# Optimization experiments

Hardware: AMD Instinct MI355X
Metric: run time of the kernel (lower is better)

Reference implementation:

```python
import jax, jax.numpy as jnp
import numpy as np

D = 512       # d_model
H = 8         # n_heads
HD = D // H   # head_dim = 64
BS = 64       # block_size
B = 1
S = 8192
NB = S // BS  # 128 blocks
THRESH = 0.3


def setup_inputs() -> dict:
    key = jax.random.key(0)
    ks = jax.random.split(key, 6)
    sc = 0.02
    return {
        "x": jax.random.normal(ks[0], (B, S, D), jnp.float32),
        "w_qkv": (jax.random.normal(ks[1], (D, 3 * D)) * sc).astype(jnp.float32),
        "b_qkv": jnp.zeros((3 * D,), jnp.float32),
        "w_out": (jax.random.normal(ks[2], (D, D)) * sc).astype(jnp.float32),
        "b_out": jnp.zeros((D,), jnp.float32),
        "w_r1": (jax.random.normal(ks[3], (D, 128)) * sc).astype(jnp.float32),
        "b_r1": jnp.zeros((128,), jnp.float32),
        "w_r2": (jax.random.normal(ks[4], (128, 1)) * sc).astype(jnp.float32),
        "b_r2": jnp.full((1,), 0.5, jnp.float32),  # sigmoid(~0.5)>0.3 -> non-degenerate mask
    }


def reference(x, w_qkv, b_qkv, w_out, b_out, w_r1, b_r1, w_r2, b_r2):
    Bx, Sx, Dx = x.shape
    qkv = (x @ w_qkv + b_qkv).reshape(Bx, Sx, 3, H, HD)
    q = jnp.transpose(qkv[:, :, 0], (0, 2, 1, 3))  # [B,H,S,HD]
    k = jnp.transpose(qkv[:, :, 1], (0, 2, 1, 3))
    v = jnp.transpose(qkv[:, :, 2], (0, 2, 1, 3))

    # --- router: per-block importance from mean-pooled q block (d_model features) ---
    qb = q.reshape(Bx, H, NB, BS, HD)
    rep = jnp.transpose(qb.mean(axis=3), (0, 2, 1, 3)).reshape(Bx, NB, Dx)  # [B,NB,D]
    imp = jax.nn.sigmoid(jax.nn.relu(rep @ w_r1 + b_r1) @ w_r2 + b_r2)[..., 0]  # [B,NB]
    keep = (imp.mean(axis=0) >= THRESH).astype(x.dtype)  # [NB], shared across batch (torch uses batch-mean)

    kb = k.reshape(Bx, H, NB, BS, HD)
    vb = v.reshape(Bx, H, NB, BS, HD)
    tri = jnp.triu(jnp.ones((BS, BS), bool), 1)  # strict upper triangle within diagonal block
    jidx = jnp.arange(NB)
    scale = 1.0 / np.sqrt(HD)

    def step(carry, i):
        q_i = jax.lax.dynamic_slice_in_dim(q, i * BS, BS, axis=2)        # [B,H,BSq,HD]
        s = jnp.einsum('bhqd,bhjkd->bhqjk', q_i, kb) * scale             # [B,H,BSq,NB,BSk]
        causal = (jidx == i)[None, :, None] & tri[:, None, :]            # [BSq,NB,BSk]
        s = jnp.where(causal[None, None], -jnp.inf, s)
        p = jax.nn.softmax(s, axis=-1)                                   # softmax PER key-block (as in torch loop)
        wj = keep * keep[i]                                              # block pair gate [NB]
        o = jnp.einsum('bhqjk,j,bhjkd->bhqd', p, wj, vb)                 # sum of gated per-block contributions
        return carry, o

    _, outs = jax.lax.scan(step, None, jnp.arange(NB))                   # [NB,B,H,BSq,HD]
    attn = jnp.transpose(outs, (1, 2, 0, 3, 4)).reshape(Bx, H, Sx, HD)
    attn = jnp.transpose(attn, (0, 2, 1, 3)).reshape(Bx, Sx, Dx)
    return attn @ w_out + b_out
```

## Files before the change

kernel.cpp:

```cpp
#include <hip/hip_runtime.h>

typedef unsigned short u16;
typedef unsigned int u32;
typedef __attribute__((ext_vector_type(8))) short short8;
typedef __attribute__((ext_vector_type(4))) short short4v;
typedef __attribute__((ext_vector_type(4))) float f32x4;
typedef __attribute__((ext_vector_type(4))) float float4v;
typedef __attribute__((ext_vector_type(2))) u32 u32x2;
typedef __attribute__((ext_vector_type(4))) u32 u32x4;

#define S_LEN 8192
#define NHEAD 8
#define NBLK  128
#define SCALE_C 0.18033688011112042f

__device__ __forceinline__ u16 f2b(float f) {
    union { float f; unsigned u; } v; v.f = f;
    unsigned r = v.u + 0x7FFFu + ((v.u >> 16) & 1u);
    return (u16)(r >> 16);
}
__device__ __forceinline__ float b2f(u16 b) {
    union { float f; unsigned u; } v; v.u = ((unsigned)b) << 16; return v.f;
}
__device__ __forceinline__ u32 cvt_pk_bf16(float lo, float hi) {
    u32 r;
    asm("v_cvt_pk_bf16_f32 %0, %1, %2" : "=v"(r) : "v"(lo), "v"(hi));
    return r;
}
__device__ __forceinline__ void pl16swap(u32& a, u32& b) {
    u32x2 r = __builtin_amdgcn_permlane16_swap(a, b, false, false);
    a = r[0]; b = r[1];
}
__device__ __forceinline__ void pl32swap(u32& a, u32& b) {
    u32x2 r = __builtin_amdgcn_permlane32_swap(a, b, false, false);
    a = r[0]; b = r[1];
}
__device__ __forceinline__ int swz(int row, int colByte) {
    return row * 128 + (colByte ^ ((row & 7) << 4));
}
__device__ __forceinline__ void gload_lds(const void* g, void* l) {
    __builtin_amdgcn_global_load_lds(
        (const __attribute__((address_space(1))) void*)g,
        (__attribute__((address_space(3))) void*)l, 16, 0, 0);
}

__global__ __launch_bounds__(256) void cvt_x_kernel(const float* __restrict__ x, u16* __restrict__ xb) {
    int idx = blockIdx.x * 256 + threadIdx.x;
    float4v v = *((const float4v*)x + idx);
    short4v o;
    #pragma unroll
    for (int r = 0; r < 4; ++r) o[r] = (short)f2b(v[r]);
    *((short4v*)xb + idx) = o;
}

__global__ __launch_bounds__(256) void cvt_T_kernel(const float* __restrict__ w, u16* __restrict__ wt, int C) {
    int idx = blockIdx.x * 256 + threadIdx.x;
    int r = idx & 511, cc = idx >> 9;
    wt[idx] = f2b(w[(size_t)r * C + cc]);
}

__global__ __launch_bounds__(256) void sum4_kernel(const u16* __restrict__ a0, const u16* __restrict__ a1,
                                                   const u16* __restrict__ a2, const u16* __restrict__ a3,
                                                   int n, u16* __restrict__ outb) {
    int idx = blockIdx.x * 256 + threadIdx.x;
    short8 v0 = ((const short8*)a0)[idx];
    short8 v1 = ((const short8*)a1)[idx];
    float s[8];
    #pragma unroll
    for (int e = 0; e < 8; ++e) s[e] = b2f((u16)v0[e]) + b2f((u16)v1[e]);
    if (n == 4) {
        short8 v2 = ((const short8*)a2)[idx];
        short8 v3 = ((const short8*)a3)[idx];
        #pragma unroll
        for (int e = 0; e < 8; ++e) s[e] += b2f((u16)v2[e]) + b2f((u16)v3[e]);
    }
    short8 o;
    #pragma unroll
    for (int e = 0; e < 8; ++e) o[e] = (short)f2b(s[e]);
    ((short8*)outb)[idx] = o;
}

__device__ __forceinline__ void gemm128_core(const u16* __restrict__ A,
                                             const u16* __restrict__ Bt,
                                             int m0, int n0, char* As, char* Bs,
                                             f32x4 acc[4][4]) {
    const int tid = threadIdx.x;
    const int lane = tid & 63, wid = tid >> 6;
    const int q16 = lane >> 4, l16 = lane & 15;
    const int wm = wid >> 1, wn = wid & 1;
    #pragma unroll 1
    for (int kt = 0; kt < 8; ++kt) {
        const int k0 = kt * 64;
        __syncthreads();
        #pragma unroll
        for (int p = 0; p < 4; ++p) {
            int c = tid + p * 256;
            int row = c >> 3, colp = (c & 7) ^ (row & 7);
            gload_lds(A  + (size_t)(m0 + row) * 512 + k0 + colp * 8, As + (size_t)(wid * 64 + p * 256) * 16);
            gload_lds(Bt + (size_t)(n0 + row) * 512 + k0 + colp * 8, Bs + (size_t)(wid * 64 + p * 256) * 16);
        }
        __syncthreads();
        #pragma unroll
        for (int kk = 0; kk < 2; ++kk) {
            short8 a[4], b[4];
            #pragma unroll
            for (int t = 0; t < 4; ++t) {
                int arow = wm * 64 + t * 16 + l16;
                a[t] = *(const short8*)(As + swz(arow, kk * 64 + q16 * 16));
                int brow = wn * 64 + t * 16 + l16;
                b[t] = *(const short8*)(Bs + swz(brow, kk * 64 + q16 * 16));
            }
            #pragma unroll
            for (int mt = 0; mt < 4; ++mt)
                #pragma unroll
                for (int nt = 0; nt < 4; ++nt)
                    acc[mt][nt] = __builtin_amdgcn_mfma_f32_16x16x32_bf16(a[mt], b[nt], acc[mt][nt], 0, 0, 0);
        }
    }
}

__global__ __launch_bounds__(256) void qkv_gemm(const u16* __restrict__ xb, const u16* __restrict__ wqkvT,
                                                const float* __restrict__ bqkv,
                                                u16* __restrict__ qb, u16* __restrict__ kf, u16* __restrict__ vf) {
    __shared__ char smem[32768];
    f32x4 acc[4][4];
    #pragma unroll
    for (int a = 0; a < 4; ++a)
        #pragma unroll
        for (int b = 0; b < 4; ++b) acc[a][b] = (f32x4){0.f, 0.f, 0.f, 0.f};
    const int m0 = blockIdx.x * 128, n0 = blockIdx.y * 128;
    gemm128_core(xb, wqkvT, m0, n0, smem, smem + 16384, acc);

    const int lane = threadIdx.x & 63, wid = threadIdx.x >> 6;
    const int q16 = lane >> 4, l16 = lane & 15;
    const int wm = wid >> 1, wn = wid & 1;
    #pragma unroll
    for (int mt = 0; mt < 4; ++mt) {
        #pragma unroll
        for (int nt = 0; nt < 4; ++nt) {
            int n = n0 + wn * 64 + nt * 16 + l16;
            float bias = bqkv[n];
            int t = n >> 9, h = (n >> 6) & 7, d = n & 63;
            int sb = m0 + wm * 64 + mt * 16 + q16 * 4;
            f32x4 v = acc[mt][nt];
            if (t == 0) {
                #pragma unroll
                for (int r = 0; r < 4; ++r)
                    qb[(size_t)(h * S_LEN + sb + r) * 64 + d] = f2b((v[r] + bias) * SCALE_C);
            } else if (t == 1) {
                int j = sb >> 6, key = sb & 63;
                int n0k = key >> 4, c = d >> 5, q16k = (d >> 3) & 3, e = d & 7;
                int ub = (n0k * 2 + c) * 64 + q16k * 16 + (key & 15);
                u16* base = kf + (size_t)h * 524288 + (size_t)j * 4096 + e;
                #pragma unroll
                for (int r = 0; r < 4; ++r)
                    base[(ub + r) * 8] = f2b(v[r] + bias);
            } else {
                int j = sb >> 6, key = sb & 63;
                int dt = d >> 4, c = key >> 5, q16v = (key >> 3) & 3, e0 = key & 7;
                int u = (dt * 2 + c) * 64 + q16v * 16 + (d & 15);
                short4v pk;
                #pragma unroll
                for (int r = 0; r < 4; ++r) pk[r] = (short)f2b(v[r] + bias);
                *(short4v*)(vf + (size_t)h * 524288 + (size_t)j * 4096 + u * 8 + e0) = pk;
            }
        }
    }
}

__global__ __launch_bounds__(256) void out_gemm(const u16* __restrict__ a0, const u16* __restrict__ wotT,
                                                const float* __restrict__ bout, float* __restrict__ out) {
    __shared__ char smem[32768];
    f32x4 acc[4][4];
    #pragma unroll
    for (int a = 0; a < 4; ++a)
        #pragma unroll
        for (int b = 0; b < 4; ++b) acc[a][b] = (f32x4){0.f, 0.f, 0.f, 0.f};
    const int m0 = blockIdx.x * 128, n0 = blockIdx.y * 128;
    gemm128_core(a0, wotT, m0, n0, smem, smem + 16384, acc);

    const int lane = threadIdx.x & 63, wid = threadIdx.x >> 6;
    const int q16 = lane >> 4, l16 = lane & 15;
    const int wm = wid >> 1, wn = wid & 1;
    #pragma unroll
    for (int mt = 0; mt < 4; ++mt) {
        #pragma unroll
        for (int nt = 0; nt < 4; ++nt) {
            int n = n0 + wn * 64 + nt * 16 + l16;
            float bias = bout[n];
            int sb = m0 + wm * 64 + mt * 16 + q16 * 4;
            #pragma unroll
            for (int r = 0; r < 4; ++r)
                out[(size_t)(sb + r) * 512 + n] = acc[mt][nt][r] + bias;
        }
    }
}

__global__ __launch_bounds__(256) void router_kernel(const u16* __restrict__ qb,
                                                     const float* __restrict__ w_r1, const float* __restrict__ b_r1,
                                                     const float* __restrict__ w_r2, const float* __restrict__ b_r2,
                                                     float* __restrict__ keepf) {
    const int nb = blockIdx.x, tid = threadIdx.x;
    __shared__ float rep[512];
    __shared__ float h1[128];
    for (int dim = tid; dim < 512; dim += 256) {
        int h = dim >> 6, d = dim & 63;
        const u16* p = qb + (size_t)(h * S_LEN + nb * 64) * 64 + d;
        float s = 0.f;
        #pragma unroll 4
        for (int t = 0; t < 64; ++t) s += b2f(p[t * 64]);
        rep[dim] = s * (0.015625f / SCALE_C);
    }
    __syncthreads();
    if (tid < 128) {
        float a = b_r1[tid];
        for (int k = 0; k < 512; ++k) a += rep[k] * w_r1[k * 128 + tid];
        h1[tid] = fmaxf(a, 0.f);
    }
    __syncthreads();
    if (tid < 64) {
        float v = h1[tid] * w_r2[tid] + h1[tid + 64] * w_r2[tid + 64];
        #pragma unroll
        for (int off = 32; off; off >>= 1) v += __shfl_down(v, off);
        if (tid == 0) {
            float z = v + b_r2[0];
            keepf[nb] = (z >= -0.84729786f) ? 1.0f : 0.0f;
        }
    }
}

__global__ __launch_bounds__(256, 4) void attn_kernel(const u16* __restrict__ qb, const u16* __restrict__ kf,
                                                      const u16* __restrict__ vf, const float* __restrict__ keepf,
                                                      u16* __restrict__ a0, u16* __restrict__ a1,
                                                      u16* __restrict__ a2, u16* __restrict__ a3, int nj) {
    const int i = blockIdx.x, h = blockIdx.y, jh = blockIdx.z;
    const int j0 = jh * nj;
    u16* __restrict__ att = (jh == 0) ? a0 : (jh == 1) ? a1 : (jh == 2) ? a2 : a3;
    const int tid = threadIdx.x, lane = tid & 63, wid = tid >> 6;
    const int q16 = lane >> 4, l16 = lane & 15;
    __shared__ char smem[40960];

    short8 bq[2][2];
    #pragma unroll
    for (int qh = 0; qh < 2; ++qh) {
        const u16* qrow = qb + (size_t)(h * S_LEN + i * 128 + wid * 32 + qh * 16 + l16) * 64;
        bq[qh][0] = *(const short8*)(qrow + q16 * 8);
        bq[qh][1] = *(const short8*)(qrow + 32 + q16 * 8);
    }
    const int kq_s = __builtin_amdgcn_readfirstlane(i * 2 + (wid >> 1));
    const float keep_i = keepf[kq_s];
    const u32 kvbits = __builtin_bit_cast(u32, keepf[(j0 + lane) & 127]);
    const int qloc = (wid & 1) * 32 + l16;

    f32x4 o[2][4];
    #pragma unroll
    for (int qh = 0; qh < 2; ++qh)
        #pragma unroll
        for (int t = 0; t < 4; ++t) o[qh][t] = (f32x4){0.f, 0.f, 0.f, 0.f};

    const int lb = lane * 16;
    const int stoff = (wid * 128 + lane) * 8;
    const int ldw = wid * 2048;

    const u16* kst = kf + (size_t)h * 524288 + stoff + (size_t)j0 * 4096;
    const u16* vst = vf + (size_t)h * 524288 + stoff + (size_t)j0 * 4096;
    char *kRead = smem + 8192, *kStage = smem;
    char *vPV = smem + 16384, *vNext = smem + 24576, *vStage = smem + 32768;

    asm volatile("s_waitcnt vmcnt(0)" ::: "memory");

    auto STAGE = [&](char* kdst, char* vdst) {
        gload_lds(kst,       kdst + ldw);   gload_lds(kst + 512, kdst + ldw + 1024);
        gload_lds(vst,       vdst + ldw);   gload_lds(vst + 512, vdst + ldw + 1024);
        kst += 4096; vst += 4096;
    };
    auto QK = [&](const char* Kc, f32x4 (&s)[2][4]) {
        __builtin_amdgcn_s_setprio(1);
        #pragma unroll
        for (int n0 = 0; n0 < 4; ++n0) {
            short8 ka0 = *(const short8*)(Kc + n0 * 2048 + lb);
            short8 ka1 = *(const short8*)(Kc + n0 * 2048 + 1024 + lb);
            #pragma unroll
            for (int qh = 0; qh < 2; ++qh) {
                f32x4 a = (f32x4){0.f, 0.f, 0.f, 0.f};
                a = __builtin_amdgcn_mfma_f32_16x16x32_bf16(ka0, bq[qh][0], a, 0, 0, 0);
                a = __builtin_amdgcn_mfma_f32_16x16x32_bf16(ka1, bq[qh][1], a, 0, 0, 0);
                s[qh][n0] = a;
            }
        }
        __builtin_amdgcn_s_setprio(0);
    };
    auto SMPV = [&](int jjl, const f32x4 (&s)[2][4], const char* Vc) {
        const float kj = __builtin_bit_cast(float, (u32)__builtin_amdgcn_readlane((int)kvbits, jjl));
        const float gj = keep_i * kj;
        const int j = j0 + jjl;
        short8 pb[2][2];
        #pragma unroll
        for (int qh = 0; qh < 2; ++qh) {
            f32x4 p4[4];
            #pragma unroll
            for (int n0 = 0; n0 < 4; ++n0)
                #pragma unroll
                for (int r = 0; r < 4; ++r)
                    p4[n0][r] = __builtin_amdgcn_exp2f(s[qh][n0][r]);
            if (j == kq_s) {
                const int qthis = qloc + qh * 16;
                #pragma unroll
                for (int n0 = 0; n0 < 4; ++n0)
                    #pragma unroll
                    for (int r = 0; r < 4; ++r)
                        if (n0 * 16 + q16 * 4 + r > qthis) p4[n0][r] = 0.f;
            }
            f32x4 sv = (p4[0] + p4[1]) + (p4[2] + p4[3]);
            float sum = (sv[0] + sv[1]) + (sv[2] + sv[3]);
            {
                u32 sa = __builtin_bit_cast(u32, sum), sb = sa;
                pl16swap(sa, sb);
                sum = __builtin_bit_cast(float, sa) + __builtin_bit_cast(float, sb);
                u32 sc = __builtin_bit_cast(u32, sum), sd = sc;
                pl32swap(sc, sd);
                sum = __builtin_bit_cast(float, sc) + __builtin_bit_cast(float, sd);
            }
            const float rinv = gj * __builtin_amdgcn_rcpf(sum);
            u32 dw[4][2];
            #pragma unroll
            for (int n0 = 0; n0 < 4; ++n0) {
                f32x4 t = p4[n0] * rinv;
                dw[n0][0] = cvt_pk_bf16(t[0], t[1]);
                dw[n0][1] = cvt_pk_bf16(t[2], t[3]);
            }
            #pragma unroll
            for (int kk = 0; kk < 2; ++kk) {
                u32 c0 = dw[2 * kk][0], d0 = dw[2 * kk + 1][0];
                pl32swap(c0, d0);
                pl16swap(c0, d0);
                u32 c1 = dw[2 * kk][1], d1 = dw[2 * kk + 1][1];
                pl32swap(c1, d1);
                pl16swap(c1, d1);
                u32x4 wv;
                wv[0] = c0; wv[1] = c1; wv[2] = d0; wv[3] = d1;
                pb[qh][kk] = __builtin_bit_cast(short8, wv);
            }
        }
        __builtin_amdgcn_s_setprio(1);
        #pragma unroll
        for (int dt = 0; dt < 4; ++dt) {
            short8 va0 = *(const short8*)(Vc + dt * 2048 + lb);
            short8 va1 = *(const short8*)(Vc + dt * 2048 + 1024 + lb);
            #pragma unroll
            for (int qh = 0; qh < 2; ++qh) {
                o[qh][dt] = __builtin_amdgcn_mfma_f32_16x16x32_bf16(va0, pb[qh][0], o[qh][dt], 0, 0, 0);
                o[qh][dt] = __builtin_amdgcn_mfma_f32_16x16x32_bf16(va1, pb[qh][1], o[qh][dt], 0, 0, 0);
            }
        }
        __builtin_amdgcn_s_setprio(0);
    };
    auto WAITBAR = [&]() {
        asm volatile("s_waitcnt vmcnt(0)" ::: "memory");
        __builtin_amdgcn_s_barrier();
        __builtin_amdgcn_sched_barrier(0);
    };
    auto ROT = [&]() {
        char* t = kRead; kRead = kStage; kStage = t;
        char* u = vPV; vPV = vNext; vNext = vStage; vStage = u;
    };

    STAGE(kStage, vPV);
    STAGE(kRead, vNext);
    asm volatile("s_waitcnt vmcnt(4)" ::: "memory");
    __builtin_amdgcn_s_barrier();

    f32x4 sA[2][4], sB[2][4];
    QK(kStage, sA);

    for (int jj = 0; jj + 3 < nj; jj += 2) {
        WAITBAR();
        STAGE(kStage, vStage);
        QK(kRead, sB);
        SMPV(jj, sA, vPV);
        ROT();
        WAITBAR();
        STAGE(kStage, vStage);
        QK(kRead, sA);
        SMPV(jj + 1, sB, vPV);
        ROT();
    }
    WAITBAR();
    QK(kRead, sB);
    SMPV(nj - 2, sA, vPV);
    ROT();
    WAITBAR();
    SMPV(nj - 1, sB, vPV);

    #pragma unroll
    for (int qh = 0; qh < 2; ++qh) {
        u16* obase = att + (size_t)(i * 128 + wid * 32 + qh * 16 + l16) * 512 + h * 64 + q16 * 4;
        #pragma unroll
        for (int dt = 0; dt < 4; ++dt) {
            u32x2 st;
            st[0] = cvt_pk_bf16(o[qh][dt][0], o[qh][dt][1]);
            st[1] = cvt_pk_bf16(o[qh][dt][2], o[qh][dt][3]);
            *(u32x2*)(obase + dt * 16) = st;
        }
    }
}

static const size_t OFF_WQKVT = 0;
static const size_t OFF_WOTT  = (size_t)2u << 20;
static const size_t OFF_KEEP  = ((size_t)2u << 20) + (512u << 10);
static const size_t OFF_QB    = (size_t)3u << 20;
static const size_t OFF_KF    = (size_t)11u << 20;
static const size_t OFF_VF    = (size_t)19u << 20;
static const size_t OFF_XB    = (size_t)27u << 20;
static const size_t OFF_P0    = (size_t)35u << 20;
static const size_t OFF_P1    = (size_t)43u << 20;
static const size_t OFF_P2    = (size_t)51u << 20;

extern "C" void kernel_launch(void* const* d_in, const int* in_sizes, int n_in,
                              void* d_out, int out_size, void* d_ws, size_t ws_size,
                              hipStream_t stream) {
    const float* x     = (const float*)d_in[0];
    const float* w_qkv = (const float*)d_in[1];
    const float* b_qkv = (const float*)d_in[2];
    const float* w_out = (const float*)d_in[3];
    const float* b_out = (const float*)d_in[4];
    const float* w_r1  = (const float*)d_in[5];
    const float* b_r1  = (const float*)d_in[6];
    const float* w_r2  = (const float*)d_in[7];
    const float* b_r2  = (const float*)d_in[8];
    float* out = (float*)d_out;
    char* ws = (char*)d_ws;
    u16* wqkvT  = (u16*)(ws + OFF_WQKVT);
    u16* wotT   = (u16*)(ws + OFF_WOTT);
    float* keepf = (float*)(ws + OFF_KEEP);
    u16* qb     = (u16*)(ws + OFF_QB);
    u16* kf     = (u16*)(ws + OFF_KF);
    u16* vf     = (u16*)(ws + OFF_VF);
    u16* xb     = (u16*)(ws + OFF_XB);
    u16* attnb  = (u16*)(ws + OFF_QB);

    const bool big = ws_size >= ((size_t)59u << 20) + 4096;
    const int njh = big ? 4 : 2;
    const int nj  = NBLK / njh;
    u16* a0 = (u16*)(ws + OFF_P0);
    u16* a1 = big ? (u16*)(ws + OFF_P1) : (u16*)(ws + OFF_XB);
    u16* a2 = big ? (u16*)(ws + OFF_P2) : a0;
    u16* a3 = big ? (u16*)(ws + OFF_XB) : a0;

    cvt_x_kernel<<<4096, 256, 0, stream>>>(x, xb);
    cvt_T_kernel<<<3072, 256, 0, stream>>>(w_qkv, wqkvT, 1536);
    cvt_T_kernel<<<1024, 256, 0, stream>>>(w_out, wotT, 512);
    qkv_gemm<<<dim3(64, 12), 256, 0, stream>>>(xb, wqkvT, b_qkv, qb, kf, vf);
    router_kernel<<<128, 256, 0, stream>>>(qb, w_r1, b_r1, w_r2, b_r2, keepf);
    attn_kernel<<<dim3(64, 8, njh), 256, 0, stream>>>(qb, kf, vf, keepf, a0, a1, a2, a3, nj);
    sum4_kernel<<<2048, 256, 0, stream>>>(a0, a1, a2, a3, njh, attnb);
    out_gemm<<<dim3(64, 4), 256, 0, stream>>>(attnb, wotT, b_out, out);
}
```

Measured before the change: 240.5 us.

## Shrink attention LDS to 2-deep V ring, fix 2-way key split, vectorize router

The attention kernel now keeps two V buffers in LDS instead of three, cutting shared memory from 40KB to 32KB and raising the launch bound to 5 blocks per CU. It always splits the key range into two halves instead of four when the workspace is large, and it reorders the grid so heads and key halves vary fastest. The router now reduces each query block with 16-byte vector loads and a partial-sum table, and the final combine adds only two partial outputs. In exchange there is less V prefetch depth and fewer blocks in flight for the larger workspace configuration.

```diff
diff --git a/kernel.cpp b/kernel.cpp
--- a/kernel.cpp
+++ b/kernel.cpp
@@ -59,24 +59,14 @@
     wt[idx] = f2b(w[(size_t)r * C + cc]);
 }
 
-__global__ __launch_bounds__(256) void sum4_kernel(const u16* __restrict__ a0, const u16* __restrict__ a1,
-                                                   const u16* __restrict__ a2, const u16* __restrict__ a3,
-                                                   int n, u16* __restrict__ outb) {
+__global__ __launch_bounds__(256) void sum2_kernel(const u16* __restrict__ a0, const u16* __restrict__ a1,
+                                                   u16* __restrict__ outb) {
     int idx = blockIdx.x * 256 + threadIdx.x;
     short8 v0 = ((const short8*)a0)[idx];
     short8 v1 = ((const short8*)a1)[idx];
-    float s[8];
-    #pragma unroll
-    for (int e = 0; e < 8; ++e) s[e] = b2f((u16)v0[e]) + b2f((u16)v1[e]);
-    if (n == 4) {
-        short8 v2 = ((const short8*)a2)[idx];
-        short8 v3 = ((const short8*)a3)[idx];
-        #pragma unroll
-        for (int e = 0; e < 8; ++e) s[e] += b2f((u16)v2[e]) + b2f((u16)v3[e]);
-    }
     short8 o;
     #pragma unroll
-    for (int e = 0; e < 8; ++e) o[e] = (short)f2b(s[e]);
+    for (int e = 0; e < 8; ++e) o[e] = (short)f2b(b2f((u16)v0[e]) + b2f((u16)v1[e]));
     ((short8*)outb)[idx] = o;
 }
 
@@ -201,16 +191,25 @@
                                                      const float* __restrict__ w_r2, const float* __restrict__ b_r2,
                                                      float* __restrict__ keepf) {
     const int nb = blockIdx.x, tid = threadIdx.x;
+    __shared__ float part[512][4];
     __shared__ float rep[512];
     __shared__ float h1[128];
-    for (int dim = tid; dim < 512; dim += 256) {
-        int h = dim >> 6, d = dim & 63;
-        const u16* p = qb + (size_t)(h * S_LEN + nb * 64) * 64 + d;
-        float s = 0.f;
+    {
+        int h = tid >> 5, rs = (tid >> 3) & 3, g = tid & 7;
+        const u16* base = qb + (size_t)(h * S_LEN + nb * 64 + rs * 16) * 64 + g * 8;
+        float acc[8] = {0.f, 0.f, 0.f, 0.f, 0.f, 0.f, 0.f, 0.f};
         #pragma unroll 4
-        for (int t = 0; t < 64; ++t) s += b2f(p[t * 64]);
-        rep[dim] = s * (0.015625f / SCALE_C);
-    }
+        for (int r = 0; r < 16; ++r) {
+            short8 v = *(const short8*)(base + (size_t)r * 64);
+            #pragma unroll
+            for (int e = 0; e < 8; ++e) acc[e] += b2f((u16)v[e]);
+        }
+        #pragma unroll
+        for (int e = 0; e < 8; ++e) part[h * 64 + g * 8 + e][rs] = acc[e];
+    }
+    __syncthreads();
+    for (int dim = tid; dim < 512; dim += 256)
+        rep[dim] = (part[dim][0] + part[dim][1] + part[dim][2] + part[dim][3]) * (0.015625f / SCALE_C);
     __syncthreads();
     if (tid < 128) {
         float a = b_r1[tid];
@@ -229,16 +228,15 @@
     }
 }
 
-__global__ __launch_bounds__(256, 4) void attn_kernel(const u16* __restrict__ qb, const u16* __restrict__ kf,
+__global__ __launch_bounds__(256, 5) void attn_kernel(const u16* __restrict__ qb, const u16* __restrict__ kf,
                                                       const u16* __restrict__ vf, const float* __restrict__ keepf,
-                                                      u16* __restrict__ a0, u16* __restrict__ a1,
-                                                      u16* __restrict__ a2, u16* __restrict__ a3, int nj) {
-    const int i = blockIdx.x, h = blockIdx.y, jh = blockIdx.z;
+                                                      u16* __restrict__ a0, u16* __restrict__ a1, int nj) {
+    const int h = blockIdx.x, jh = blockIdx.y, i = blockIdx.z;
     const int j0 = jh * nj;
-    u16* __restrict__ att = (jh == 0) ? a0 : (jh == 1) ? a1 : (jh == 2) ? a2 : a3;
+    u16* __restrict__ att = jh ? a1 : a0;
     const int tid = threadIdx.x, lane = tid & 63, wid = tid >> 6;
     const int q16 = lane >> 4, l16 = lane & 15;
-    __shared__ char smem[40960];
+    __shared__ char smem[32768];
 
     short8 bq[2][2];
     #pragma unroll
@@ -264,15 +262,18 @@
 
     const u16* kst = kf + (size_t)h * 524288 + stoff + (size_t)j0 * 4096;
     const u16* vst = vf + (size_t)h * 524288 + stoff + (size_t)j0 * 4096;
-    char *kRead = smem + 8192, *kStage = smem;
-    char *vPV = smem + 16384, *vNext = smem + 24576, *vStage = smem + 32768;
+    char *kStage = smem, *kRead = smem + 8192;
+    char *vCur = smem + 16384, *vStage = smem + 24576;
 
     asm volatile("s_waitcnt vmcnt(0)" ::: "memory");
 
-    auto STAGE = [&](char* kdst, char* vdst) {
-        gload_lds(kst,       kdst + ldw);   gload_lds(kst + 512, kdst + ldw + 1024);
-        gload_lds(vst,       vdst + ldw);   gload_lds(vst + 512, vdst + ldw + 1024);
-        kst += 4096; vst += 4096;
+    auto STAGE_K = [&](char* dst) {
+        gload_lds(kst, dst + ldw);   gload_lds(kst + 512, dst + ldw + 1024);
+        kst += 4096;
+    };
+    auto STAGE_V = [&](char* dst) {
+        gload_lds(vst, dst + ldw);   gload_lds(vst + 512, dst + ldw + 1024);
+        vst += 4096;
     };
     auto QK = [&](const char* Kc, f32x4 (&s)[2][4]) {
         __builtin_amdgcn_s_setprio(1);
@@ -362,12 +363,13 @@
     };
     auto ROT = [&]() {
         char* t = kRead; kRead = kStage; kStage = t;
-        char* u = vPV; vPV = vNext; vNext = vStage; vStage = u;
-    };
-
-    STAGE(kStage, vPV);
-    STAGE(kRead, vNext);
-    asm volatile("s_waitcnt vmcnt(4)" ::: "memory");
+        char* u = vCur; vCur = vStage; vStage = u;
+    };
+
+    STAGE_K(kStage);
+    STAGE_V(vCur);
+    STAGE_K(kRead);
+    asm volatile("s_waitcnt vmcnt(2)" ::: "memory");
     __builtin_amdgcn_s_barrier();
 
     f32x4 sA[2][4], sB[2][4];
@@ -375,22 +377,25 @@
 
     for (int jj = 0; jj + 3 < nj; jj += 2) {
         WAITBAR();
-        STAGE(kStage, vStage);
+        STAGE_K(kStage);
+        STAGE_V(vStage);
         QK(kRead, sB);
-        SMPV(jj, sA, vPV);
+        SMPV(jj, sA, vCur);
         ROT();
         WAITBAR();
-        STAGE(kStage, vStage);
+        STAGE_K(kStage);
+        STAGE_V(vStage);
         QK(kRead, sA);
-        SMPV(jj + 1, sB, vPV);
+        SMPV(jj + 1, sB, vCur);
         ROT();
     }
     WAITBAR();
+    STAGE_V(vStage);
     QK(kRead, sB);
-    SMPV(nj - 2, sA, vPV);
+    SMPV(nj - 2, sA, vCur);
     ROT();
     WAITBAR();
-    SMPV(nj - 1, sB, vPV);
+    SMPV(nj - 1, sB, vCur);
 
     #pragma unroll
     for (int qh = 0; qh < 2; ++qh) {
@@ -413,8 +418,6 @@
 static const size_t OFF_VF    = (size_t)19u << 20;
 static const size_t OFF_XB    = (size_t)27u << 20;
 static const size_t OFF_P0    = (size_t)35u << 20;
-static const size_t OFF_P1    = (size_t)43u << 20;
-static const size_t OFF_P2    = (size_t)51u << 20;
 
 extern "C" void kernel_launch(void* const* d_in, const int* in_sizes, int n_in,
                               void* d_out, int out_size, void* d_ws, size_t ws_size,
@@ -438,21 +441,15 @@
     u16* vf     = (u16*)(ws + OFF_VF);
     u16* xb     = (u16*)(ws + OFF_XB);
     u16* attnb  = (u16*)(ws + OFF_QB);
-
-    const bool big = ws_size >= ((size_t)59u << 20) + 4096;
-    const int njh = big ? 4 : 2;
-    const int nj  = NBLK / njh;
-    u16* a0 = (u16*)(ws + OFF_P0);
-    u16* a1 = big ? (u16*)(ws + OFF_P1) : (u16*)(ws + OFF_XB);
-    u16* a2 = big ? (u16*)(ws + OFF_P2) : a0;
-    u16* a3 = big ? (u16*)(ws + OFF_XB) : a0;
+    u16* a0     = (u16*)(ws + OFF_P0);
+    u16* a1     = (u16*)(ws + OFF_XB);
 
     cvt_x_kernel<<<4096, 256, 0, stream>>>(x, xb);
     cvt_T_kernel<<<3072, 256, 0, stream>>>(w_qkv, wqkvT, 1536);
     cvt_T_kernel<<<1024, 256, 0, stream>>>(w_out, wotT, 512);
     qkv_gemm<<<dim3(64, 12), 256, 0, stream>>>(xb, wqkvT, b_qkv, qb, kf, vf);
     router_kernel<<<128, 256, 0, stream>>>(qb, w_r1, b_r1, w_r2, b_r2, keepf);
-    attn_kernel<<<dim3(64, 8, njh), 256, 0, stream>>>(qb, kf, vf, keepf, a0, a1, a2, a3, nj);
-    sum4_kernel<<<2048, 256, 0, stream>>>(a0, a1, a2, a3, njh, attnb);
+    attn_kernel<<<dim3(8, 2, 64), 256, 0, stream>>>(qb, kf, vf, keepf, a0, a1, 64);
+    sum2_kernel<<<2048, 256, 0, stream>>>(a0, a1, attnb);
     out_gemm<<<dim3(64, 4), 256, 0, stream>>>(attnb, wotT, b_out, out);
 }
```

New measurement: 674.3 us. 2.8x slower.
